# Optimization experiments

Measured on AMD Instinct MI355X. Metric: run time of the kernel, lower is better.

## Reference

```python
import jax, jax.numpy as jnp
import numpy as np
import math

G = 8        # groups
ORDER = 2    # Taylor order
GAMMA = 1e-4 # RBF gamma
EPS = 1e-5   # GroupNorm eps


def setup_inputs() -> dict:
    key = jax.random.key(0)
    ks = jax.random.split(key, 6)
    B, C_HI, C_LO, P = 16, 512, 512, 256
    H1 = W1 = 64
    H2 = W2 = 32
    s = 0.02
    return {
        "input_high": jax.random.normal(ks[0], (B, C_HI, H1, W1), jnp.float32),
        "input_low": jax.random.normal(ks[1], (B, C_LO, H2, W2), jnp.float32),
        "Wt": jax.random.normal(ks[2], (P, C_HI), jnp.float32) * s,
        "Wp": jax.random.normal(ks[3], (P, C_LO), jnp.float32) * s,
        "Wg": jax.random.normal(ks[4], (P, C_LO), jnp.float32) * s,
        # grouped 1x1 conv planes -> inplanes1: [G, out_per_group, in_per_group]
        "Wz": jax.random.normal(ks[5], (G, C_HI // G, P // G), jnp.float32) * s,
        "gn_w": jnp.ones((C_HI,), jnp.float32),
        "gn_b": jnp.zeros((C_HI,), jnp.float32),
    }


def _taylor_alpha():
    # alpha_k = sqrt((2*gamma)^k / k! * exp(-2*gamma)) for k = 0..ORDER
    ks = np.arange(ORDER + 1)
    fact = np.array([math.factorial(int(k)) for k in ks], dtype=np.float64)
    a = np.sqrt((2.0 * GAMMA) ** ks / fact * np.exp(-2.0 * GAMMA))
    return jnp.asarray(a, jnp.float32)


def reference(input_high, input_low, Wt, Wp, Wg, Wz, gn_w, gn_b):
    # 1x1-conv projections as channel contractions
    t = jnp.einsum('bchw,oc->bohw', input_high, Wt)   # [b, P, h1, w1]
    p = jnp.einsum('bchw,oc->bohw', input_low, Wp)    # [b, P, h2, w2]
    g = jnp.einsum('bchw,oc->bohw', input_low, Wg)    # [b, P, h2, w2]
    b, c1, h1, w1 = t.shape

    alpha = _taylor_alpha()                            # [ORDER+1]
    # split channels into groups, flatten (c/G)*h*w per group
    tg = t.reshape(b, G, -1)                           # [b, G, N1]
    pg = p.reshape(b, G, -1)                           # [b, G, N2]
    gg = g.reshape(b, G, -1)                           # [b, G, N2]

    # low-rank Taylor feature maps: [b, G, ORDER+1, N]
    t_tay = jnp.stack([tg ** k for k in range(ORDER + 1)], axis=2) * alpha[None, None, :, None]
    p_tay = jnp.stack([pg ** k for k in range(ORDER + 1)], axis=2) * alpha[None, None, :, None]

    att = jnp.einsum('bgkn,bgn->bgk', p_tay, gg)       # [b, G, ORDER+1]
    x = jnp.einsum('bgk,bgkn->bgn', att, t_tay)        # [b, G, N1]
    x = x.reshape(b, G, c1 // G, h1, w1)               # grouped feature map

    # grouped 1x1 conv z: planes -> inplanes1
    z = jnp.einsum('bgihw,goi->bgohw', x, Wz)
    z = z.reshape(b, -1, h1, w1)                       # [b, C_HI, h1, w1]

    # GroupNorm(num_groups=G) with affine, then residual
    zg = z.reshape(b, G, -1)
    mu = zg.mean(axis=-1, keepdims=True)
    var = zg.var(axis=-1, keepdims=True)
    zn = ((zg - mu) * jax.lax.rsqrt(var + EPS)).reshape(z.shape)
    out = zn * gn_w[None, :, None, None] + gn_b[None, :, None, None] + input_high
    return out
```

## Files before the change

kernel.cpp:

```cpp
#include <hip/hip_runtime.h>
#include <math.h>

typedef __attribute__((ext_vector_type(8))) short short8;
typedef __attribute__((ext_vector_type(8))) unsigned short u16x8;
typedef __attribute__((ext_vector_type(4))) float f32x4;

#define EPS_ 1e-5f

__device__ inline unsigned int cvtpk(float a, float b) {
    unsigned int r;
    asm("v_cvt_pk_bf16_f32 %0, %1, %2" : "=v"(r) : "v"(a), "v"(b));
    return r;
}

__device__ inline f32x4 mfma16(u16x8 a, u16x8 b, f32x4 c) {
    return __builtin_amdgcn_mfma_f32_16x16x32_bf16((short8)a, (short8)b, c, 0, 0, 0);
}

__device__ inline void gll16(const unsigned short* g, unsigned short* l) {
    __builtin_amdgcn_global_load_lds(
        (const __attribute__((address_space(1))) unsigned int*)g,
        (__attribute__((address_space(3))) unsigned int*)l, 16, 0, 0);
}

__global__ __launch_bounds__(256)
void k0s(const float* __restrict__ xlo, float* __restrict__ sxsum)
{
    __shared__ float sred[256];
    int blk = blockIdx.x;
    int cgrp = blk & 15, b = blk >> 4;
    int tid = threadIdx.x;
    int cl = tid >> 3, seg = tid & 7;
    int c = cgrp * 32 + cl;
    const float* row = xlo + ((size_t)b * 512 + c) * 1024 + seg * 128;
    float s = 0.f;
#pragma unroll
    for (int i = 0; i < 32; i++) {
        float4 v = ((const float4*)row)[i];
        s += v.x + v.y + v.z + v.w;
    }
    sred[tid] = s;
    __syncthreads();
    if (seg == 0) {
        float t = 0.f;
#pragma unroll
        for (int e = 0; e < 8; e++) t += sred[cl * 8 + e];
        sxsum[(size_t)b * 512 + c] = t;
    }
}

__global__ __launch_bounds__(256)
void k0w_t(const float* __restrict__ Wt, unsigned short* __restrict__ wtb)
{
    int blk = blockIdx.x, tid = threadIdx.x;
    int kc = blk >> 3, sub = blk & 7;
    int idx = sub * 256 + tid;
    int row = idx >> 3, s = idx & 7;
    int colbase = kc * 64 + ((s ^ (row & 7)) << 3);
    const float* sp = Wt + (size_t)row * 512 + colbase;
    float4 v0 = ((const float4*)sp)[0];
    float4 v1 = ((const float4*)sp)[1];
    uint4 q = { cvtpk(v0.x, v0.y), cvtpk(v0.z, v0.w),
                cvtpk(v1.x, v1.y), cvtpk(v1.z, v1.w) };
    *(uint4*)&wtb[(size_t)(kc * 2048 + idx) * 8] = q;
}

#define K1_BODY(C0, VCUR, VNXT, DOPREF)                                          \
  {                                                                              \
    if (DOPREF) {                                                                \
        const float* xc = xlo + ((size_t)b * 512 + (C0) + 64 + cs * 8) * 1024 + hw0 + xrow; \
        _Pragma("unroll")                                                        \
        for (int j = 0; j < 8; j++) VNXT[j] = xc[(size_t)j * 1024];              \
    }                                                                            \
    __syncthreads();                                                             \
    _Pragma("unroll")                                                            \
    for (int k = 0; k < 4; k++) {                                                \
        int idx = k * 256 + tid;                                                 \
        int row = idx >> 3, s = idx & 7;                                         \
        const float* pp = Wp + (size_t)(pbase + row) * 512 + (C0) + s * 8;       \
        const float* pg = Wg + (size_t)(pbase + row) * 512 + (C0) + s * 8;       \
        float4 a0 = ((const float4*)pp)[0], a1 = ((const float4*)pp)[1];         \
        float4 b0 = ((const float4*)pg)[0], b1 = ((const float4*)pg)[1];         \
        uint4 qp = { cvtpk(a0.x,a0.y), cvtpk(a0.z,a0.w),                         \
                     cvtpk(a1.x,a1.y), cvtpk(a1.z,a1.w) };                       \
        uint4 qg = { cvtpk(b0.x,b0.y), cvtpk(b0.z,b0.w),                         \
                     cvtpk(b1.x,b1.y), cvtpk(b1.z,b1.w) };                       \
        int off = row * 64 + ((s ^ (row & 7)) << 3);                             \
        *(uint4*)&sWp[off] = qp;                                                 \
        *(uint4*)&sWg[off] = qg;                                                 \
    }                                                                            \
    {                                                                            \
        uint4 q = { cvtpk(VCUR[0],VCUR[1]), cvtpk(VCUR[2],VCUR[3]),              \
                    cvtpk(VCUR[4],VCUR[5]), cvtpk(VCUR[6],VCUR[7]) };            \
        int phys = cs ^ (xrow & 7);                                              \
        *(uint4*)&sX1[xrow * 64 + phys * 8] = q;                                 \
    }                                                                            \
    __syncthreads();                                                             \
    _Pragma("unroll")                                                            \
    for (int kk = 0; kk < 2; kk++) {                                             \
        u16x8 bf[2];                                                             \
        _Pragma("unroll")                                                        \
        for (int ht = 0; ht < 2; ht++) {                                         \
            int row = ht * 16 + l15;                                             \
            bf[ht] = *(const u16x8*)&sX1[row * 64 + (((kk*4+l4) ^ (row&7)) << 3)]; \
        }                                                                        \
        _Pragma("unroll")                                                        \
        for (int i = 0; i < 2; i++) {                                            \
            int row = w * 32 + i * 16 + l15;                                     \
            int off = row * 64 + (((kk*4+l4) ^ (row&7)) << 3);                   \
            u16x8 ap = *(const u16x8*)&sWp[off];                                 \
            u16x8 ag = *(const u16x8*)&sWg[off];                                 \
            _Pragma("unroll")                                                    \
            for (int ht = 0; ht < 2; ht++) {                                     \
                pacc[i][ht] = mfma16(ap, bf[ht], pacc[i][ht]);                   \
                gacc[i][ht] = mfma16(ag, bf[ht], gacc[i][ht]);                   \
            }                                                                    \
        }                                                                        \
    }                                                                            \
  }

__global__ __launch_bounds__(256, 4)
void k1_att(const float* __restrict__ xlo, const float* __restrict__ Wp,
            const float* __restrict__ Wg, float* __restrict__ att_part)
{
    __shared__ unsigned short sWp[8192];
    __shared__ unsigned short sWg[8192];
    __shared__ unsigned short sX1[2048];

    int tid = threadIdx.x;
    int w = tid >> 6, lane = tid & 63;
    int l15 = lane & 15, l4 = lane >> 4;
    int beta = blockIdx.x;
    int tile = beta & 31, mh = (beta >> 5) & 1, b = beta >> 6;
    int hw0 = tile * 32;
    int pbase = mh * 128;
    int xrow = tid & 31, cs = tid >> 5;

    f32x4 pacc[2][2] = {};
    f32x4 gacc[2][2] = {};

    float vbA[8], vbB[8];
    {
        const float* xc = xlo + ((size_t)b * 512 + cs * 8) * 1024 + hw0 + xrow;
#pragma unroll
        for (int j = 0; j < 8; j++) vbA[j] = xc[(size_t)j * 1024];
    }

    for (int kc2 = 0; kc2 < 4; kc2++) {
        int c0 = kc2 * 128;
        K1_BODY(c0,      vbA, vbB, true);
        K1_BODY(c0 + 64, vbB, vbA, (kc2 < 3));
    }

    float s1 = 0.f, s2 = 0.f;
#pragma unroll
    for (int i = 0; i < 2; i++)
#pragma unroll
        for (int ht = 0; ht < 2; ht++)
#pragma unroll
            for (int r = 0; r < 4; r++) {
                float pv = pacc[i][ht][r], gv = gacc[i][ht][r];
                s1 += pv * gv; s2 += pv * pv * gv;
            }
#pragma unroll
    for (int m = 1; m < 64; m <<= 1) {
        s1 += __shfl_xor(s1, m);
        s2 += __shfl_xor(s2, m);
    }
    if (lane == 0) {
        int g = mh * 4 + w;
        float* dst = att_part + ((size_t)(b * 8 + g) * 32 + tile) * 2;
        dst[0] = s1; dst[1] = s2;
    }
}

__global__ __launch_bounds__(64)
void k1b_coef(const float* __restrict__ Wg, const float* __restrict__ sxsum,
              const float* __restrict__ att_part, float* __restrict__ coef,
              float a0s, float a1s, float a2s)
{
    int bg = blockIdx.x;
    int b = bg >> 3, g = bg & 7;
    int l = threadIdx.x;
    float s0 = 0.f;
    for (int cc = 0; cc < 512; cc += 64) {
        int c = cc + l;
        float cs = 0.f;
#pragma unroll
        for (int pp = 0; pp < 32; pp++) cs += Wg[(size_t)(g * 32 + pp) * 512 + c];
        s0 += cs * sxsum[(size_t)b * 512 + c];
    }
    float s1 = (l < 32) ? att_part[((size_t)bg * 32 + l) * 2 + 0] : 0.f;
    float s2 = (l < 32) ? att_part[((size_t)bg * 32 + l) * 2 + 1] : 0.f;
#pragma unroll
    for (int m = 1; m < 64; m <<= 1) {
        s0 += __shfl_xor(s0, m);
        s1 += __shfl_xor(s1, m);
        s2 += __shfl_xor(s2, m);
    }
    if (l == 0) {
        coef[bg * 3 + 0] = a0s * s0;
        coef[bg * 3 + 1] = a1s * s1;
        coef[bg * 3 + 2] = a2s * s2;
    }
}

#define XLOAD(DST, KC)                                                           \
  { const float* xc = xhi + ((size_t)(b * 512 + (KC) * 64 + w * 8)) * 4096 + hw0 + xrow; \
    _Pragma("unroll")                                                            \
    for (int j = 0; j < 8; j++) DST[j] = xc[(size_t)j * 4096]; }

#define K2NCHUNK(KC, WBUF, PBUF, DOGLL, DOPREF, ENDVMC)                          \
  {                                                                              \
                     \
    int row0 = w * 32 + l15, row1 = w * 32 + 16 + l15;                           \
    u16x8 af0 = *(const u16x8*)&sWt[row0 * 64 + (((0 + l4) ^ (row0 & 7)) << 3)]; \
    u16x8 af1 = *(const u16x8*)&sWt[row1 * 64 + (((0 + l4) ^ (row1 & 7)) << 3)]; \
    u16x8 af2 = *(const u16x8*)&sWt[row0 * 64 + (((4 + l4) ^ (row0 & 7)) << 3)]; \
    u16x8 af3 = *(const u16x8*)&sWt[row1 * 64 + (((4 + l4) ^ (row1 & 7)) << 3)]; \
                    \
    asm volatile("s_waitcnt vmcnt(0)" ::: "memory");                             \
    __builtin_amdgcn_sched_barrier(0);                                           \
    {                                                                            \
        uint4 q = { cvtpk(WBUF[0],WBUF[1]), cvtpk(WBUF[2],WBUF[3]),              \
                    cvtpk(WBUF[4],WBUF[5]), cvtpk(WBUF[6],WBUF[7]) };            \
        int phys = w ^ (xrow & 7);                                               \
        *(uint4*)&sX[(((KC)+1)&1) * 4096 + xrow * 64 + phys * 8] = q;            \
    }                                                                            \
    asm volatile("s_waitcnt lgkmcnt(0)" ::: "memory");                           \
    __builtin_amdgcn_s_barrier();                                                \
    __builtin_amdgcn_sched_barrier(0);                                           \
    if (DOGLL) {                                                                 \
        _Pragma("unroll")                                                        \
        for (int k = 0; k < 4; k++) {                                            \
            int u = k * 512 + tid;                                               \
            gll16(wtb + (((size_t)((KC)+1) * 2048 + u) << 3), &sWt[u << 3]);     \
        }                                                                        \
    }                                                                            \
    if (DOPREF) { XLOAD(PBUF, (KC)+2) }                                          \
    __builtin_amdgcn_sched_barrier(0);                                           \
    __builtin_amdgcn_s_setprio(1);                                               \
    _Pragma("unroll")                                                            \
    for (int kk = 0; kk < 2; kk++) {                                             \
        u16x8 bf[4];                                                             \
        _Pragma("unroll")                                                        \
        for (int ht = 0; ht < 4; ht++) {                                         \
            int row = ht * 16 + l15;                                             \
            bf[ht] = *(const u16x8*)&sX[((KC)&1) * 4096 + row * 64 + (((kk*4+l4) ^ (row&7)) << 3)]; \
        }                                                                        \
        _Pragma("unroll")                                                        \
        for (int ht = 0; ht < 4; ht++) {                                         \
            acc[0][ht] = mfma16(kk == 0 ? af0 : af2, bf[ht], acc[0][ht]);        \
            acc[1][ht] = mfma16(kk == 0 ? af1 : af3, bf[ht], acc[1][ht]);        \
        }                                                                        \
    }                                                                            \
    __builtin_amdgcn_s_setprio(0);                                               \
    asm volatile("s_waitcnt vmcnt(" #ENDVMC ")" ::: "memory");                   \
    __builtin_amdgcn_s_barrier();                                                \
    __builtin_amdgcn_sched_barrier(0);                                           \
  }

__global__ __launch_bounds__(512, 4)
void k2_main_g(const float* __restrict__ xhi, const unsigned short* __restrict__ wtb,
               const float* __restrict__ Wz, const float* __restrict__ coef,
               float* __restrict__ zout, float* __restrict__ zstat)
{
    __shared__ unsigned short sWt[16384];
    __shared__ unsigned short sX[8192];

    int tid = threadIdx.x;
    int w = tid >> 6, lane = tid & 63;
    int l15 = lane & 15, l4 = lane >> 4;
    int hwt = blockIdx.x & 63, b = blockIdx.x >> 6;
    int hw0 = hwt * 64;
    int xrow = tid & 63;

    const float* cf = coef + (size_t)(b * 8 + w) * 3;
    float c0v = cf[0], c1v = cf[1], c2v = cf[2];

    f32x4 acc[2][4] = {};

    float vA[8], vB[8];
    {
#pragma unroll
        for (int k = 0; k < 4; k++) {
            int u = k * 512 + tid;
            gll16(wtb + ((size_t)u << 3), &sWt[u << 3]);
        }
        XLOAD(vA, 0)
        XLOAD(vB, 1)
        asm volatile("s_waitcnt vmcnt(8)" ::: "memory");
        __builtin_amdgcn_s_barrier();
        __builtin_amdgcn_sched_barrier(0);
        uint4 q = { cvtpk(vA[0],vA[1]), cvtpk(vA[2],vA[3]),
                    cvtpk(vA[4],vA[5]), cvtpk(vA[6],vA[7]) };
        int phys = w ^ (xrow & 7);
        *(uint4*)&sX[xrow * 64 + phys * 8] = q;
    }

    K2NCHUNK(0, vB, vA, 1, 1, 8)
    K2NCHUNK(1, vA, vB, 1, 1, 8)
    K2NCHUNK(2, vB, vA, 1, 1, 8)
    K2NCHUNK(3, vA, vB, 1, 1, 8)
    K2NCHUNK(4, vB, vA, 1, 1, 8)
    K2NCHUNK(5, vA, vB, 1, 1, 8)
    K2NCHUNK(6, vB, vA, 1, 0, 0)
    {
        int row0 = w * 32 + l15, row1 = w * 32 + 16 + l15;
        u16x8 af0 = *(const u16x8*)&sWt[row0 * 64 + (((0 + l4) ^ (row0 & 7)) << 3)];
        u16x8 af1 = *(const u16x8*)&sWt[row1 * 64 + (((0 + l4) ^ (row1 & 7)) << 3)];
        u16x8 af2 = *(const u16x8*)&sWt[row0 * 64 + (((4 + l4) ^ (row0 & 7)) << 3)];
        u16x8 af3 = *(const u16x8*)&sWt[row1 * 64 + (((4 + l4) ^ (row1 & 7)) << 3)];
#pragma unroll
        for (int kk = 0; kk < 2; kk++) {
            u16x8 bf[4];
#pragma unroll
            for (int ht = 0; ht < 4; ht++) {
                int row = ht * 16 + l15;
                bf[ht] = *(const u16x8*)&sX[4096 + row * 64 + (((kk*4+l4) ^ (row&7)) << 3)];
            }
#pragma unroll
            for (int ht = 0; ht < 4; ht++) {
                acc[0][ht] = mfma16(kk == 0 ? af0 : af2, bf[ht], acc[0][ht]);
                acc[1][ht] = mfma16(kk == 0 ? af1 : af3, bf[ht], acc[1][ht]);
            }
        }
    }

#pragma unroll
    for (int i = 0; i < 2; i++)
#pragma unroll
        for (int ht = 0; ht < 4; ht++) {
            f32x4 t = acc[i][ht];
            acc[i][ht] = c1v * t + c2v * t * t;
        }
    __syncthreads();

#pragma unroll
    for (int i = 0; i < 2; i++)
#pragma unroll
        for (int ht = 0; ht < 4; ht++) {
            int row = ht * 16 + l15;
            f32x4 xv = acc[i][ht];
            uint2 q = { cvtpk(xv[0], xv[1]), cvtpk(xv[2], xv[3]) };
            int phys = w * 4 + ((i * 2 + (l4 >> 1)) ^ (row & 3));
            *(uint2*)&sWt[row * 256 + phys * 8 + (l4 & 1) * 4] = q;
        }

    float* sR = (float*)sX;
    {
        const float* wr = Wz + (size_t)tid * 32;
        float s = 0.f;
#pragma unroll
        for (int q = 0; q < 8; q++) {
            float4 v = ((const float4*)wr)[q];
            s += v.x + v.y + v.z + v.w;
        }
        sR[tid] = s;
    }
    u16x8 wzf[4];
#pragma unroll
    for (int ot = 0; ot < 4; ot++) {
        const float* wr = Wz + (size_t)(w * 64 + ot * 16 + l15) * 32 + l4 * 8;
        float4 v0 = ((const float4*)wr)[0];
        float4 v1 = ((const float4*)wr)[1];
        uint4 q = { cvtpk(v0.x,v0.y), cvtpk(v0.z,v0.w),
                    cvtpk(v1.x,v1.y), cvtpk(v1.z,v1.w) };
        wzf[ot] = *(u16x8*)&q;
    }
    __syncthreads();

    float s = 0.f, s2a = 0.f;
    f32x4 zero4 = {0.f, 0.f, 0.f, 0.f};
#pragma unroll
    for (int ht = 0; ht < 4; ht++) {
        int row = ht * 16 + l15;
        u16x8 bfr = *(const u16x8*)&sWt[row * 256 + (w * 4 + (l4 ^ (row & 3))) * 8];
#pragma unroll
        for (int ot = 0; ot < 4; ot++) {
            f32x4 z = mfma16(wzf[ot], bfr, zero4);
            f32x4 rv = *(const f32x4*)&sR[w * 64 + ot * 16 + l4 * 4];
            z = z + c0v * rv;
            float* zp = zout + ((size_t)(b * 512 + w * 64 + ot * 16 + l4 * 4)) * 4096
                      + hw0 + ht * 16 + l15;
#pragma unroll
            for (int r = 0; r < 4; r++) {
                zp[(size_t)r * 4096] = z[r];
                s += z[r]; s2a += z[r] * z[r];
            }
        }
    }
#pragma unroll
    for (int m = 1; m < 64; m <<= 1) {
        s   += __shfl_xor(s, m);
        s2a += __shfl_xor(s2a, m);
    }
    if (lane == 0) {
        atomicAdd(&zstat[(size_t)(b * 8 + w) * 2 + 0], s);
        atomicAdd(&zstat[(size_t)(b * 8 + w) * 2 + 1], s2a);
    }
}

#define K2_BODY(C0, VCUR, VNXT, DOPREF)                                          \
  {                                                                              \
    if (DOPREF) {                                                                \
        const float* xc = xhi + ((size_t)b * 512 + (C0) + 64 + w * 8) * 4096 + hw0 + xrow; \
        _Pragma("unroll")                                                        \
        for (int j = 0; j < 8; j++) VNXT[j] = xc[(size_t)j * 4096];              \
    }                                                                            \
    __syncthreads();                                                             \
    _Pragma("unroll")                                                            \
    for (int k = 0; k < 4; k++) {                                                \
        int idx = k * 512 + tid;                                                 \
        int row = idx >> 3, s = idx & 7;                                         \
        const float* sp = Wt + (size_t)row * 512 + (C0) + s * 8;                 \
        float4 v0 = ((const float4*)sp)[0];                                      \
        float4 v1 = ((const float4*)sp)[1];                                      \
        uint4 q = { cvtpk(v0.x,v0.y), cvtpk(v0.z,v0.w),                          \
                    cvtpk(v1.x,v1.y), cvtpk(v1.z,v1.w) };                        \
        *(uint4*)&sWt[row * 64 + ((s ^ (row & 7)) << 3)] = q;                    \
    }                                                                            \
    {                                                                            \
        uint4 q = { cvtpk(VCUR[0],VCUR[1]), cvtpk(VCUR[2],VCUR[3]),              \
                    cvtpk(VCUR[4],VCUR[5]), cvtpk(VCUR[6],VCUR[7]) };            \
        int phys = w ^ (xrow & 7);                                               \
        *(uint4*)&sX[xrow * 64 + phys * 8] = q;                                  \
    }                                                                            \
    __syncthreads();                                                             \
    _Pragma("unroll")                                                            \
    for (int kk = 0; kk < 2; kk++) {                                             \
        u16x8 bf[4];                                                             \
        _Pragma("unroll")                                                        \
        for (int ht = 0; ht < 4; ht++) {                                         \
            int row = ht * 16 + l15;                                             \
            bf[ht] = *(const u16x8*)&sX[row * 64 + (((kk*4+l4) ^ (row&7)) << 3)]; \
        }                                                                        \
        _Pragma("unroll")                                                        \
        for (int i = 0; i < 2; i++) {                                            \
            int row = w * 32 + i * 16 + l15;                                     \
            u16x8 af = *(const u16x8*)&sWt[row * 64 + (((kk*4+l4) ^ (row&7)) << 3)]; \
            _Pragma("unroll")                                                    \
            for (int ht = 0; ht < 4; ht++)                                       \
                acc[i][ht] = mfma16(af, bf[ht], acc[i][ht]);                     \
        }                                                                        \
    }                                                                            \
  }

__global__ __launch_bounds__(512, 4)
void k2_main_fb(const float* __restrict__ xhi, const float* __restrict__ Wt,
                const float* __restrict__ Wz, const float* __restrict__ coef,
                float* __restrict__ zout, float* __restrict__ zstat)
{
    __shared__ unsigned short sWt[16384];
    __shared__ unsigned short sX[8192];

    int tid = threadIdx.x;
    int w = tid >> 6, lane = tid & 63;
    int l15 = lane & 15, l4 = lane >> 4;
    int hwt = blockIdx.x & 63, b = blockIdx.x >> 6;
    int hw0 = hwt * 64;
    int xrow = tid & 63;

    const float* cf = coef + (size_t)(b * 8 + w) * 3;
    float c0v = cf[0], c1v = cf[1], c2v = cf[2];

    f32x4 acc[2][4] = {};

    float vbA[8], vbB[8];
    {
        const float* xc = xhi + ((size_t)b * 512 + w * 8) * 4096 + hw0 + xrow;
#pragma unroll
        for (int j = 0; j < 8; j++) vbA[j] = xc[(size_t)j * 4096];
    }

    for (int kc2 = 0; kc2 < 4; kc2++) {
        int c0 = kc2 * 128;
        K2_BODY(c0,      vbA, vbB, true);
        K2_BODY(c0 + 64, vbB, vbA, (kc2 < 3));
    }

#pragma unroll
    for (int i = 0; i < 2; i++)
#pragma unroll
        for (int ht = 0; ht < 4; ht++) {
            f32x4 t = acc[i][ht];
            acc[i][ht] = c1v * t + c2v * t * t;
        }
    __syncthreads();
#pragma unroll
    for (int i = 0; i < 2; i++)
#pragma unroll
        for (int ht = 0; ht < 4; ht++) {
            int row = ht * 16 + l15;
            f32x4 xv = acc[i][ht];
            uint2 q = { cvtpk(xv[0], xv[1]), cvtpk(xv[2], xv[3]) };
            int phys = w * 4 + ((i * 2 + (l4 >> 1)) ^ (row & 3));
            *(uint2*)&sWt[row * 256 + phys * 8 + (l4 & 1) * 4] = q;
        }
    float* sR = (float*)sX;
    {
        const float* wr = Wz + (size_t)tid * 32;
        float s = 0.f;
#pragma unroll
        for (int q = 0; q < 8; q++) {
            float4 v = ((const float4*)wr)[q];
            s += v.x + v.y + v.z + v.w;
        }
        sR[tid] = s;
    }
    u16x8 wzf[4];
#pragma unroll
    for (int ot = 0; ot < 4; ot++) {
        const float* wr = Wz + (size_t)(w * 64 + ot * 16 + l15) * 32 + l4 * 8;
        float4 v0 = ((const float4*)wr)[0];
        float4 v1 = ((const float4*)wr)[1];
        uint4 q = { cvtpk(v0.x,v0.y), cvtpk(v0.z,v0.w),
                    cvtpk(v1.x,v1.y), cvtpk(v1.z,v1.w) };
        wzf[ot] = *(u16x8*)&q;
    }
    __syncthreads();

    float s = 0.f, s2a = 0.f;
    f32x4 zero4 = {0.f, 0.f, 0.f, 0.f};
#pragma unroll
    for (int ht = 0; ht < 4; ht++) {
        int row = ht * 16 + l15;
        u16x8 bfr = *(const u16x8*)&sWt[row * 256 + (w * 4 + (l4 ^ (row & 3))) * 8];
#pragma unroll
        for (int ot = 0; ot < 4; ot++) {
            f32x4 z = mfma16(wzf[ot], bfr, zero4);
            f32x4 rv = *(const f32x4*)&sR[w * 64 + ot * 16 + l4 * 4];
            z = z + c0v * rv;
            float* zp = zout + ((size_t)(b * 512 + w * 64 + ot * 16 + l4 * 4)) * 4096
                      + hw0 + ht * 16 + l15;
#pragma unroll
            for (int r = 0; r < 4; r++) {
                zp[(size_t)r * 4096] = z[r];
                s += z[r]; s2a += z[r] * z[r];
            }
        }
    }
#pragma unroll
    for (int m = 1; m < 64; m <<= 1) {
        s   += __shfl_xor(s, m);
        s2a += __shfl_xor(s2a, m);
    }
    if (lane == 0) {
        atomicAdd(&zstat[(size_t)(b * 8 + w) * 2 + 0], s);
        atomicAdd(&zstat[(size_t)(b * 8 + w) * 2 + 1], s2a);
    }
}

__global__ void k2b_gn(const float* __restrict__ zstat, float* __restrict__ gnstat)
{
    int t = threadIdx.x;
    if (t >= 128) return;
    float S = zstat[t * 2], S2 = zstat[t * 2 + 1];
    const float N = 64.0f * 4096.0f;
    float mean = S / N;
    float var = S2 / N - mean * mean;
    var = var < 0.f ? 0.f : var;
    gnstat[t * 2] = mean;
    gnstat[t * 2 + 1] = rsqrtf(var + EPS_);
}

__global__ __launch_bounds__(256)
void k3_final(float* __restrict__ out, const float* __restrict__ xhi,
              const float* __restrict__ gnstat, const float* __restrict__ gnw,
              const float* __restrict__ gnb)
{
#pragma unroll
    for (int k = 0; k < 4; k++) {
        size_t idx = (size_t)blockIdx.x * 1024 + (size_t)k * 256 + threadIdx.x;
        size_t e = idx * 4;
        int ch = (int)((e >> 12) & 511);
        int b  = (int)(e >> 21);
        int gg = ch >> 6;
        const float* gs = gnstat + (size_t)(b * 8 + gg) * 2;
        float mean = gs[0];
        float w = gnw[ch] * gs[1];
        float bb = gnb[ch];
        float4 z = ((const float4*)out)[idx];
        float4 xv = ((const float4*)xhi)[idx];
        float4 r;
        r.x = (z.x - mean) * w + bb + xv.x;
        r.y = (z.y - mean) * w + bb + xv.y;
        r.z = (z.z - mean) * w + bb + xv.z;
        r.w = (z.w - mean) * w + bb + xv.w;
        ((float4*)out)[idx] = r;
    }
}

extern "C" void kernel_launch(void* const* d_in, const int* in_sizes, int n_in,
                              void* d_out, int out_size, void* d_ws, size_t ws_size,
                              hipStream_t stream) {
    (void)in_sizes; (void)n_in; (void)out_size;
    const float* xhi = (const float*)d_in[0];
    const float* xlo = (const float*)d_in[1];
    const float* Wt  = (const float*)d_in[2];
    const float* Wp  = (const float*)d_in[3];
    const float* Wg  = (const float*)d_in[4];
    const float* Wz  = (const float*)d_in[5];
    const float* gnw = (const float*)d_in[6];
    const float* gnb = (const float*)d_in[7];
    float* out = (float*)d_out;
    float* ws  = (float*)d_ws;

    float* sxsum    = ws;
    float* att_part = ws + 8192;
    float* coef     = ws + 16384;
    float* zstat    = ws + 16768;
    float* gnstat   = ws + 17024;
    unsigned short* wtb = (unsigned short*)((char*)d_ws + 69632);

    const size_t WS_NEED = 69632 + 262144;
    bool use_gll = (ws_size >= WS_NEED);

    double g2 = 2.0e-4;
    double ee = exp(-g2);
    float a0s = (float)ee;
    float a1s = (float)(g2 * ee);
    float a2s = (float)(g2 * g2 * 0.5 * ee);

    k0s     <<<dim3(256),  dim3(256), 0, stream>>>(xlo, sxsum);
    k1_att  <<<dim3(1024), dim3(256), 0, stream>>>(xlo, Wp, Wg, att_part);
    k1b_coef<<<dim3(128),  dim3(64),  0, stream>>>(Wg, sxsum, att_part, coef, a0s, a1s, a2s);
    hipMemsetAsync(zstat, 0, 256 * sizeof(float), stream);
    if (use_gll) {
        k0w_t    <<<dim3(64),   dim3(256), 0, stream>>>(Wt, wtb);
        k2_main_g<<<dim3(1024), dim3(512), 0, stream>>>(xhi, wtb, Wz, coef, out, zstat);
    } else {
        k2_main_fb<<<dim3(1024), dim3(512), 0, stream>>>(xhi, Wt, Wz, coef, out, zstat);
    }
    k2b_gn  <<<dim3(1),    dim3(128), 0, stream>>>(zstat, gnstat);
    k3_final<<<dim3(8192), dim3(256), 0, stream>>>(out, xhi, gnstat, gnw, gnb);
}
```

Baseline: 207.9 us.

## Double k2 spatial tile to 128 with 1024-thread blocks to halve Wt reloads

```diff
diff --git a/kernel.cpp b/kernel.cpp
--- a/kernel.cpp
+++ b/kernel.cpp
@@ -206,35 +206,33 @@
 }
 
 #define XLOAD(DST, KC)                                                           \
-  { const float* xc = xhi + ((size_t)(b * 512 + (KC) * 64 + w * 8)) * 4096 + hw0 + xrow; \
+  { const float* xc = xhi + ((size_t)(b * 512 + (KC) * 64 + cs * 8)) * 4096 + hw0 + xrow; \
     _Pragma("unroll")                                                            \
     for (int j = 0; j < 8; j++) DST[j] = xc[(size_t)j * 4096]; }
 
 #define K2NCHUNK(KC, WBUF, PBUF, DOGLL, DOPREF, ENDVMC)                          \
   {                                                                              \
-                     \
-    int row0 = w * 32 + l15, row1 = w * 32 + 16 + l15;                           \
-    u16x8 af0 = *(const u16x8*)&sWt[row0 * 64 + (((0 + l4) ^ (row0 & 7)) << 3)]; \
-    u16x8 af1 = *(const u16x8*)&sWt[row1 * 64 + (((0 + l4) ^ (row1 & 7)) << 3)]; \
-    u16x8 af2 = *(const u16x8*)&sWt[row0 * 64 + (((4 + l4) ^ (row0 & 7)) << 3)]; \
-    u16x8 af3 = *(const u16x8*)&sWt[row1 * 64 + (((4 + l4) ^ (row1 & 7)) << 3)]; \
+           \
+    int arow = w * 16 + l15;                                                     \
+    u16x8 af0 = *(const u16x8*)&sAll[arow * 64 + (((0 + l4) ^ (arow & 7)) << 3)]; \
+    u16x8 af1 = *(const u16x8*)&sAll[arow * 64 + (((4 + l4) ^ (arow & 7)) << 3)]; \
                     \
     asm volatile("s_waitcnt vmcnt(0)" ::: "memory");                             \
     __builtin_amdgcn_sched_barrier(0);                                           \
     {                                                                            \
         uint4 q = { cvtpk(WBUF[0],WBUF[1]), cvtpk(WBUF[2],WBUF[3]),              \
                     cvtpk(WBUF[4],WBUF[5]), cvtpk(WBUF[6],WBUF[7]) };            \
-        int phys = w ^ (xrow & 7);                                               \
-        *(uint4*)&sX[(((KC)+1)&1) * 4096 + xrow * 64 + phys * 8] = q;            \
+        int phys = cs ^ (xrow & 7);                                              \
+        *(uint4*)&sAll[16384 + (((KC)+1)&1) * 8192 + xrow * 64 + phys * 8] = q;  \
     }                                                                            \
     asm volatile("s_waitcnt lgkmcnt(0)" ::: "memory");                           \
     __builtin_amdgcn_s_barrier();                                                \
     __builtin_amdgcn_sched_barrier(0);                                           \
     if (DOGLL) {                                                                 \
         _Pragma("unroll")                                                        \
-        for (int k = 0; k < 4; k++) {                                            \
-            int u = k * 512 + tid;                                               \
-            gll16(wtb + (((size_t)((KC)+1) * 2048 + u) << 3), &sWt[u << 3]);     \
+        for (int k = 0; k < 2; k++) {                                            \
+            int u = k * 1024 + tid;                                              \
+            gll16(wtb + (((size_t)((KC)+1) * 2048 + u) << 3), &sAll[u << 3]);    \
         }                                                                        \
     }                                                                            \
     if (DOPREF) { XLOAD(PBUF, (KC)+2) }                                          \
@@ -242,17 +240,15 @@
     __builtin_amdgcn_s_setprio(1);                                               \
     _Pragma("unroll")                                                            \
     for (int kk = 0; kk < 2; kk++) {                                             \
-        u16x8 bf[4];                                                             \
-        _Pragma("unroll")                                                        \
-        for (int ht = 0; ht < 4; ht++) {                                         \
+        u16x8 bf[8];                                                             \
+        _Pragma("unroll")                                                        \
+        for (int ht = 0; ht < 8; ht++) {                                         \
             int row = ht * 16 + l15;                                             \
-            bf[ht] = *(const u16x8*)&sX[((KC)&1) * 4096 + row * 64 + (((kk*4+l4) ^ (row&7)) << 3)]; \
+            bf[ht] = *(const u16x8*)&sAll[16384 + ((KC)&1) * 8192 + row * 64 + (((kk*4+l4) ^ (row&7)) << 3)]; \
         }                                                                        \
         _Pragma("unroll")                                                        \
-        for (int ht = 0; ht < 4; ht++) {                                         \
-            acc[0][ht] = mfma16(kk == 0 ? af0 : af2, bf[ht], acc[0][ht]);        \
-            acc[1][ht] = mfma16(kk == 0 ? af1 : af3, bf[ht], acc[1][ht]);        \
-        }                                                                        \
+        for (int ht = 0; ht < 8; ht++)                                           \
+            acc[ht] = mfma16(kk == 0 ? af0 : af1, bf[ht], acc[ht]);              \
     }                                                                            \
     __builtin_amdgcn_s_setprio(0);                                               \
     asm volatile("s_waitcnt vmcnt(" #ENDVMC ")" ::: "memory");                   \
@@ -260,32 +256,32 @@
     __builtin_amdgcn_sched_barrier(0);                                           \
   }
 
-__global__ __launch_bounds__(512, 4)
+__global__ __launch_bounds__(1024, 8)
 void k2_main_g(const float* __restrict__ xhi, const unsigned short* __restrict__ wtb,
                const float* __restrict__ Wz, const float* __restrict__ coef,
                float* __restrict__ zout, float* __restrict__ zstat)
 {
-    __shared__ unsigned short sWt[16384];
-    __shared__ unsigned short sX[8192];
+    __shared__ unsigned short sAll[33792];
 
     int tid = threadIdx.x;
     int w = tid >> 6, lane = tid & 63;
     int l15 = lane & 15, l4 = lane >> 4;
-    int hwt = blockIdx.x & 63, b = blockIdx.x >> 6;
-    int hw0 = hwt * 64;
-    int xrow = tid & 63;
-
-    const float* cf = coef + (size_t)(b * 8 + w) * 3;
+    int hwt = blockIdx.x & 31, b = blockIdx.x >> 5;
+    int hw0 = hwt * 128;
+    int xrow = tid & 127, cs = tid >> 7;
+    int g = w >> 1, sub = w & 1;
+
+    const float* cf = coef + (size_t)(b * 8 + g) * 3;
     float c0v = cf[0], c1v = cf[1], c2v = cf[2];
 
-    f32x4 acc[2][4] = {};
+    f32x4 acc[8] = {};
 
     float vA[8], vB[8];
     {
 #pragma unroll
-        for (int k = 0; k < 4; k++) {
-            int u = k * 512 + tid;
-            gll16(wtb + ((size_t)u << 3), &sWt[u << 3]);
+        for (int k = 0; k < 2; k++) {
+            int u = k * 1024 + tid;
+            gll16(wtb + ((size_t)u << 3), &sAll[u << 3]);
         }
         XLOAD(vA, 0)
         XLOAD(vB, 1)
@@ -294,8 +290,8 @@
         __builtin_amdgcn_sched_barrier(0);
         uint4 q = { cvtpk(vA[0],vA[1]), cvtpk(vA[2],vA[3]),
                     cvtpk(vA[4],vA[5]), cvtpk(vA[6],vA[7]) };
-        int phys = w ^ (xrow & 7);
-        *(uint4*)&sX[xrow * 64 + phys * 8] = q;
+        int phys = cs ^ (xrow & 7);
+        *(uint4*)&sAll[16384 + xrow * 64 + phys * 8] = q;
     }
 
     K2NCHUNK(0, vB, vA, 1, 1, 8)
@@ -306,49 +302,40 @@
     K2NCHUNK(5, vA, vB, 1, 1, 8)
     K2NCHUNK(6, vB, vA, 1, 0, 0)
     {
-        int row0 = w * 32 + l15, row1 = w * 32 + 16 + l15;
-        u16x8 af0 = *(const u16x8*)&sWt[row0 * 64 + (((0 + l4) ^ (row0 & 7)) << 3)];
-        u16x8 af1 = *(const u16x8*)&sWt[row1 * 64 + (((0 + l4) ^ (row1 & 7)) << 3)];
-        u16x8 af2 = *(const u16x8*)&sWt[row0 * 64 + (((4 + l4) ^ (row0 & 7)) << 3)];
-        u16x8 af3 = *(const u16x8*)&sWt[row1 * 64 + (((4 + l4) ^ (row1 & 7)) << 3)];
+        int arow = w * 16 + l15;
+        u16x8 af0 = *(const u16x8*)&sAll[arow * 64 + (((0 + l4) ^ (arow & 7)) << 3)];
+        u16x8 af1 = *(const u16x8*)&sAll[arow * 64 + (((4 + l4) ^ (arow & 7)) << 3)];
 #pragma unroll
         for (int kk = 0; kk < 2; kk++) {
-            u16x8 bf[4];
-#pragma unroll
-            for (int ht = 0; ht < 4; ht++) {
+            u16x8 bf[8];
+#pragma unroll
+            for (int ht = 0; ht < 8; ht++) {
                 int row = ht * 16 + l15;
-                bf[ht] = *(const u16x8*)&sX[4096 + row * 64 + (((kk*4+l4) ^ (row&7)) << 3)];
+                bf[ht] = *(const u16x8*)&sAll[16384 + 8192 + row * 64 + (((kk*4+l4) ^ (row&7)) << 3)];
             }
 #pragma unroll
-            for (int ht = 0; ht < 4; ht++) {
-                acc[0][ht] = mfma16(kk == 0 ? af0 : af2, bf[ht], acc[0][ht]);
-                acc[1][ht] = mfma16(kk == 0 ? af1 : af3, bf[ht], acc[1][ht]);
-            }
-        }
-    }
-
-#pragma unroll
-    for (int i = 0; i < 2; i++)
-#pragma unroll
-        for (int ht = 0; ht < 4; ht++) {
-            f32x4 t = acc[i][ht];
-            acc[i][ht] = c1v * t + c2v * t * t;
-        }
+            for (int ht = 0; ht < 8; ht++)
+                acc[ht] = mfma16(kk == 0 ? af0 : af1, bf[ht], acc[ht]);
+        }
+    }
+
+#pragma unroll
+    for (int ht = 0; ht < 8; ht++) {
+        f32x4 t = acc[ht];
+        acc[ht] = c1v * t + c2v * t * t;
+    }
     __syncthreads();
 
 #pragma unroll
-    for (int i = 0; i < 2; i++)
-#pragma unroll
-        for (int ht = 0; ht < 4; ht++) {
-            int row = ht * 16 + l15;
-            f32x4 xv = acc[i][ht];
-            uint2 q = { cvtpk(xv[0], xv[1]), cvtpk(xv[2], xv[3]) };
-            int phys = w * 4 + ((i * 2 + (l4 >> 1)) ^ (row & 3));
-            *(uint2*)&sWt[row * 256 + phys * 8 + (l4 & 1) * 4] = q;
-        }
-
-    float* sR = (float*)sX;
-    {
+    for (int ht = 0; ht < 8; ht++) {
+        int row = ht * 16 + l15;
+        f32x4 xv = acc[ht];
+        uint2 q = { cvtpk(xv[0], xv[1]), cvtpk(xv[2], xv[3]) };
+        int gran = (sub * 2 + (l4 >> 1)) ^ (row & 3);
+        *(uint2*)&sAll[row * 256 + g * 32 + gran * 8 + (l4 & 1) * 4] = q;
+    }
+    float* sR = (float*)&sAll[32768];
+    if (tid < 512) {
         const float* wr = Wz + (size_t)tid * 32;
         float s = 0.f;
 #pragma unroll
@@ -361,7 +348,7 @@
     u16x8 wzf[4];
 #pragma unroll
     for (int ot = 0; ot < 4; ot++) {
-        const float* wr = Wz + (size_t)(w * 64 + ot * 16 + l15) * 32 + l4 * 8;
+        const float* wr = Wz + (size_t)(g * 64 + ot * 16 + l15) * 32 + l4 * 8;
         float4 v0 = ((const float4*)wr)[0];
         float4 v1 = ((const float4*)wr)[1];
         uint4 q = { cvtpk(v0.x,v0.y), cvtpk(v0.z,v0.w),
@@ -373,15 +360,16 @@
     float s = 0.f, s2a = 0.f;
     f32x4 zero4 = {0.f, 0.f, 0.f, 0.f};
 #pragma unroll
-    for (int ht = 0; ht < 4; ht++) {
+    for (int htl = 0; htl < 4; htl++) {
+        int ht = sub * 4 + htl;
         int row = ht * 16 + l15;
-        u16x8 bfr = *(const u16x8*)&sWt[row * 256 + (w * 4 + (l4 ^ (row & 3))) * 8];
+        u16x8 bfr = *(const u16x8*)&sAll[row * 256 + g * 32 + ((l4 ^ (row & 3))) * 8];
 #pragma unroll
         for (int ot = 0; ot < 4; ot++) {
             f32x4 z = mfma16(wzf[ot], bfr, zero4);
-            f32x4 rv = *(const f32x4*)&sR[w * 64 + ot * 16 + l4 * 4];
+            f32x4 rv = *(const f32x4*)&sR[g * 64 + ot * 16 + l4 * 4];
             z = z + c0v * rv;
-            float* zp = zout + ((size_t)(b * 512 + w * 64 + ot * 16 + l4 * 4)) * 4096
+            float* zp = zout + ((size_t)(b * 512 + g * 64 + ot * 16 + l4 * 4)) * 4096
                       + hw0 + ht * 16 + l15;
 #pragma unroll
             for (int r = 0; r < 4; r++) {
@@ -396,8 +384,8 @@
         s2a += __shfl_xor(s2a, m);
     }
     if (lane == 0) {
-        atomicAdd(&zstat[(size_t)(b * 8 + w) * 2 + 0], s);
-        atomicAdd(&zstat[(size_t)(b * 8 + w) * 2 + 1], s2a);
+        atomicAdd(&zstat[(size_t)(b * 8 + g) * 2 + 0], s);
+        atomicAdd(&zstat[(size_t)(b * 8 + g) * 2 + 1], s2a);
     }
 }
 
@@ -627,8 +615,8 @@
     k1b_coef<<<dim3(128),  dim3(64),  0, stream>>>(Wg, sxsum, att_part, coef, a0s, a1s, a2s);
     hipMemsetAsync(zstat, 0, 256 * sizeof(float), stream);
     if (use_gll) {
-        k0w_t    <<<dim3(64),   dim3(256), 0, stream>>>(Wt, wtb);
-        k2_main_g<<<dim3(1024), dim3(512), 0, stream>>>(xhi, wtb, Wz, coef, out, zstat);
+        k0w_t    <<<dim3(64),  dim3(256),  0, stream>>>(Wt, wtb);
+        k2_main_g<<<dim3(512), dim3(1024), 0, stream>>>(xhi, wtb, Wz, coef, out, zstat);
     } else {
         k2_main_fb<<<dim3(1024), dim3(512), 0, stream>>>(xhi, Wt, Wz, coef, out, zstat);
     }
```

After: 265.1 us. 1.28x slower.
